# Performance work log

Hardware: AMD Instinct MI355X
Metric: run time of the kernel (lower is better)

## Reference

```python
import jax, jax.numpy as jnp
import numpy as np

EPS = 1e-5

def _ln(x, g, b):
    mu = jnp.mean(x, axis=-1, keepdims=True)
    var = jnp.mean((x - mu) ** 2, axis=-1, keepdims=True)
    return (x - mu) * jax.lax.rsqrt(var + EPS) * g + b

B, SQ, SK, C, H = 4, 1024, 2048, 1024, 16
DH = C // H          # head_dim (latent_dim == in_dim)
L = C                # latent_dim

def setup_inputs() -> dict:
    key = jax.random.key(0)
    ks = list(jax.random.split(key, 16))
    s = 0.02
    d = {
        'queries': jax.random.normal(ks[0], (B, SQ, C), jnp.float32),
        'contexts': jax.random.normal(ks[1], (B, SK, C), jnp.float32),
        # SelfAttention params
        'sa_ln_g': jnp.ones((C,), jnp.float32),
        'sa_ln_b': jnp.zeros((C,), jnp.float32),
        'sa_qkv_w': jax.random.normal(ks[2], (2 * L + C, C), jnp.float32) * s,  # torch Linear weight (out,in)
        'sa_out_w': jax.random.normal(ks[3], (C, C), jnp.float32) * s,
        'sa_out_b': jnp.zeros((C,), jnp.float32),
        # Cross Attention params
        'ca_ln_g': jnp.ones((C,), jnp.float32),
        'ca_ln_b': jnp.zeros((C,), jnp.float32),
        'ca_q_w': jax.random.normal(ks[4], (L, C), jnp.float32) * s,
        'ca_k_w': jax.random.normal(ks[5], (L, C), jnp.float32) * s,
        'ca_v_w': jax.random.normal(ks[6], (C, C), jnp.float32) * s,
        'ca_out_w': jax.random.normal(ks[7], (C, C), jnp.float32) * s,
        'ca_out_b': jnp.zeros((C,), jnp.float32),
        # FFN (linear block) params
        'ff_ln1_g': jnp.ones((C,), jnp.float32),
        'ff_ln1_b': jnp.zeros((C,), jnp.float32),
        'ff_w1': jax.random.normal(ks[8], (2 * C, C), jnp.float32) * s,
        'ff_ln2_g': jnp.ones((2 * C,), jnp.float32),
        'ff_ln2_b': jnp.zeros((2 * C,), jnp.float32),
        'ff_w2': jax.random.normal(ks[9], (C, 2 * C), jnp.float32) * s,
    }
    return d

def _forward(queries, contexts, sa_ln_g, sa_ln_b, sa_qkv_w, sa_out_w, sa_out_b,
             ca_ln_g, ca_ln_b, ca_q_w, ca_k_w, ca_v_w, ca_out_w, ca_out_b,
             ff_ln1_g, ff_ln1_b, ff_w1, ff_ln2_g, ff_ln2_b, ff_w2):
    scale = 1.0 / jnp.sqrt(jnp.float32(C))  # note: module scales by sqrt(C), not sqrt(head_dim)
    # ---- SelfAttention ----
    x = queries
    h = _ln(x, sa_ln_g, sa_ln_b)
    qkv = (h @ sa_qkv_w.T).reshape(B, SQ, H, -1)  # (B,SQ,H, 2*DH + C//H)
    q, k, v = jnp.split(qkv, [DH, 2 * DH], axis=-1)
    e = jnp.einsum('nqhc,nkhc->nhqk', q, k)
    a = jax.nn.softmax(e * scale, axis=-1)
    o = jnp.einsum('nhql,nlhc->nqhc', a, v).reshape(B, SQ, C)
    x = o @ sa_out_w.T + sa_out_b + x
    # ---- Cross Attention ----
    qpre = x
    hq = _ln(x, ca_ln_g, ca_ln_b)
    q = (hq @ ca_q_w.T).reshape(B, SQ, H, DH)
    k = (contexts @ ca_k_w.T).reshape(B, SK, H, DH)
    v = (contexts @ ca_v_w.T).reshape(B, SK, H, C // H)
    energy = jnp.einsum('nqhc,nkhc->nhqk', q, k)  # (B,H,SQ,SK)
    a = jax.nn.softmax(energy * scale, axis=-1)
    o = jnp.einsum('nhql,nlhc->nqhc', a, v).reshape(B, SQ, C)
    x = o @ ca_out_w.T + ca_out_b + qpre
    # ---- FFN: LN -> SiLU -> Linear -> LN -> SiLU -> Linear, residual ----
    f = jax.nn.silu(_ln(x, ff_ln1_g, ff_ln1_b))
    f = f @ ff_w1.T
    f = jax.nn.silu(_ln(f, ff_ln2_g, ff_ln2_b))
    f = f @ ff_w2.T
    out = x + f  # dropout p=0 -> identity
    return out, energy

def reference(queries, contexts, sa_ln_g, sa_ln_b, sa_qkv_w, sa_out_w, sa_out_b,
              ca_ln_g, ca_ln_b, ca_q_w, ca_k_w, ca_v_w, ca_out_w, ca_out_b,
              ff_ln1_g, ff_ln1_b, ff_w1, ff_ln2_g, ff_ln2_b, ff_w2):
    return _forward(queries, contexts, sa_ln_g, sa_ln_b, sa_qkv_w, sa_out_w, sa_out_b,
                    ca_ln_g, ca_ln_b, ca_q_w, ca_k_w, ca_v_w, ca_out_w, ca_out_b,
                    ff_ln1_g, ff_ln1_b, ff_w1, ff_ln2_g, ff_ln2_b, ff_w2)
```

## Files before the change

kernel.cpp:

```cpp
#include <hip/hip_runtime.h>
#include <hip/hip_bf16.h>
#include <math.h>


namespace {
constexpr int BB  = 4;
constexpr int SQ_ = 1024;
constexpr int SK_ = 2048;
constexpr int CC  = 1024;
constexpr int HH  = 16;
constexpr float SCALE  = 0.03125f;
constexpr float LN_EPS = 1e-5f;
constexpr size_t OPART_STRIDE = (size_t)BB * SQ_ * CC;
}

typedef __hip_bfloat16 bf16;
typedef __attribute__((ext_vector_type(8))) short short8;
typedef __attribute__((ext_vector_type(4))) float f32x4;

__device__ __forceinline__ void gload16(const void* g, void* l) {
    __builtin_amdgcn_global_load_lds((const __attribute__((address_space(1))) unsigned int*)g,
                                     (__attribute__((address_space(3))) unsigned int*)l,
                                     16, 0, 0);
}

__global__ __launch_bounds__(256)
void cvt_bf16(const float* __restrict__ in, bf16* __restrict__ out, int n8) {
    const int i = blockIdx.x * 256 + threadIdx.x;
    if (i >= n8) return;
    const float4 a = ((const float4*)in)[2 * i];
    const float4 b = ((const float4*)in)[2 * i + 1];
    union { ushort4 v; bf16 h[4]; } lo, hi;
    lo.h[0] = __float2bfloat16(a.x); lo.h[1] = __float2bfloat16(a.y);
    lo.h[2] = __float2bfloat16(a.z); lo.h[3] = __float2bfloat16(a.w);
    hi.h[0] = __float2bfloat16(b.x); hi.h[1] = __float2bfloat16(b.y);
    hi.h[2] = __float2bfloat16(b.z); hi.h[3] = __float2bfloat16(b.w);
    ((ushort4*)out)[2 * i]     = lo.v;
    ((ushort4*)out)[2 * i + 1] = hi.v;
}

template<int NCOLS>
__global__ __launch_bounds__(256)
void ln_kernel(const float* __restrict__ x, const float* __restrict__ g,
               const float* __restrict__ b, bf16* __restrict__ out, int do_silu) {
    constexpr int PER = NCOLS / 256;
    const size_t row = blockIdx.x;
    const float* xr = x + row * NCOLS;
    float vals[PER];
    float s = 0.f, ss = 0.f;
#pragma unroll
    for (int i = 0; i < PER; ++i) {
        vals[i] = xr[threadIdx.x + i * 256];
        s += vals[i];
        ss += vals[i] * vals[i];
    }
    for (int off = 32; off > 0; off >>= 1) {
        s  += __shfl_down(s, off, 64);
        ss += __shfl_down(ss, off, 64);
    }
    __shared__ float red[10];
    const int wid = threadIdx.x >> 6, lane = threadIdx.x & 63;
    if (lane == 0) { red[wid] = s; red[wid + 4] = ss; }
    __syncthreads();
    if (threadIdx.x == 0) {
        const float ts  = red[0] + red[1] + red[2] + red[3];
        const float tss = red[4] + red[5] + red[6] + red[7];
        const float mu  = ts / NCOLS;
        const float var = tss / NCOLS - mu * mu;
        red[8] = mu;
        red[9] = rsqrtf(var + LN_EPS);
    }
    __syncthreads();
    const float mu = red[8], rstd = red[9];
    bf16* outr = out + row * NCOLS;
#pragma unroll
    for (int i = 0; i < PER; ++i) {
        const int c = threadIdx.x + i * 256;
        float y = (vals[i] - mu) * rstd * g[c] + b[c];
        if (do_silu) y = y / (1.f + __expf(-y));
        outr[c] = __float2bfloat16(y);
    }
}

template<int OUT16>
__global__ __launch_bounds__(256)
void gemm_bt16(const bf16* __restrict__ A, const bf16* __restrict__ B,
               void* __restrict__ Cv, int M, int N, int K,
               const float* __restrict__ bias, const float* __restrict__ resid) {
    __shared__ bf16 As[128 * 32];
    __shared__ bf16 Bs[128 * 32];
    const int tid  = threadIdx.x;
    const int lane = tid & 63;
    const int w    = tid >> 6;
    const int wr = w >> 1, wc = w & 1;

    const int nwg = gridDim.x * gridDim.y;
    const int bid = blockIdx.x + gridDim.x * blockIdx.y;
    const int logical = (bid & 7) * (nwg >> 3) + (bid >> 3);
    const int m0 = (logical / gridDim.x) * 128;
    const int n0 = (logical % gridDim.x) * 128;

    f32x4 acc[4][4] = {};

    const int srow = tid >> 2;
    const int scol = (tid & 3) * 8;
    const bf16* Ap  = A + (size_t)(m0 + srow) * K + scol;
    const bf16* Ap2 = Ap + (size_t)64 * K;
    const bf16* Bp  = B + (size_t)(n0 + srow) * K + scol;
    const bf16* Bp2 = Bp + (size_t)64 * K;

    char* AsB = (char*)As + w * 1024;
    char* BsB = (char*)Bs + w * 1024;

    const int arow = wr * 64 + (lane & 15);
    const int brow = wc * 64 + (lane & 15);
    const int kgrp = (lane >> 4) * 16;

    for (int k0 = 0; k0 < K; k0 += 32) {
        gload16(Ap  + k0, AsB);
        gload16(Ap2 + k0, AsB + 4096);
        gload16(Bp  + k0, BsB);
        gload16(Bp2 + k0, BsB + 4096);
        __syncthreads();
        short8 aF[4], bF[4];
#pragma unroll
        for (int m = 0; m < 4; ++m)
            aF[m] = *(const short8*)((const char*)As + ((arow + m * 16) * 64 + kgrp));
#pragma unroll
        for (int n = 0; n < 4; ++n)
            bF[n] = *(const short8*)((const char*)Bs + ((brow + n * 16) * 64 + kgrp));
#pragma unroll
        for (int m = 0; m < 4; ++m)
#pragma unroll
            for (int n = 0; n < 4; ++n)
                acc[m][n] = __builtin_amdgcn_mfma_f32_16x16x32_bf16(aF[m], bF[n], acc[m][n], 0, 0, 0);
        __syncthreads();
    }

    const int crow0 = m0 + wr * 64 + (lane >> 4) * 4;
    const int ccol0 = n0 + wc * 64 + (lane & 15);
#pragma unroll
    for (int m = 0; m < 4; ++m) {
#pragma unroll
        for (int n = 0; n < 4; ++n) {
            const int col = ccol0 + n * 16;
            const float bv = (!OUT16 && bias) ? bias[col] : 0.f;
#pragma unroll
            for (int j = 0; j < 4; ++j) {
                const int row = crow0 + m * 16 + j;
                float v = acc[m][n][j] + bv;
                if (!OUT16 && resid) v += resid[(size_t)row * N + col];
                if (OUT16) ((bf16*)Cv)[(size_t)row * N + col] = __float2bfloat16(v);
                else       ((float*)Cv)[(size_t)row * N + col] = v;
            }
        }
    }
}

__global__ __launch_bounds__(256)
void transpose_v(const bf16* __restrict__ X, int ldx, int cs, int co,
                 bf16* __restrict__ T, int ldt) {
    __shared__ bf16 t[64][66];
    const int r0 = blockIdx.x * 64, c0 = blockIdx.y * 64;
#pragma unroll
    for (int s = 0; s < 16; ++s) {
        const int r = (threadIdx.x >> 6) + s * 4;
        const int c = threadIdx.x & 63;
        const int cc = c0 + c;
        t[r][c] = X[(size_t)(r0 + r) * ldx + (size_t)(cc >> 6) * cs + co + (cc & 63)];
    }
    __syncthreads();
#pragma unroll
    for (int s = 0; s < 16; ++s) {
        const int c = (threadIdx.x >> 6) + s * 4;
        const int r = threadIdx.x & 63;
        T[(size_t)(c0 + c) * ldt + r0 + r] = t[r][c];
    }
}

template<bool ENERGY, int NSPLIT>
__global__ __launch_bounds__(256, 4)
void flash_attn(const bf16* __restrict__ Qb, int ldq, int qh_str,
                const bf16* __restrict__ Kb, int ldk, int kh_str, int kh_add,
                const bf16* __restrict__ Vt, int ldvt,
                bf16* __restrict__ O, float* __restrict__ Opart,
                float* __restrict__ stats, float* __restrict__ energy,
                int SKV, int SQl, float scale) {
    __shared__ bf16 P[64][136];
    const int tid = threadIdx.x;
    const int lane = tid & 63, wid = tid >> 6;
    const int l15 = lane & 15, l4 = lane >> 4;

    const int gx  = gridDim.x;
    const int nwg = gx * gridDim.y * gridDim.z;
    const int bid = blockIdx.x + gx * (blockIdx.y + gridDim.y * blockIdx.z);
    const int logical = (bid & 7) * (nwg >> 3) + (bid >> 3);
    const int xq = logical % gx;
    const int z  = (logical / gx) % (BB * HH);
    const int split = (NSPLIT > 1) ? (logical / (gx * BB * HH)) : 0;

    const int b = z >> 4, h = z & 15;
    const int q0 = xq * 64;
    const int kv_begin = split * (SKV / NSPLIT);
    const int kv_end   = kv_begin + SKV / NSPLIT;

    const bf16* Qp = Qb + (size_t)b * SQl * ldq + (size_t)h * qh_str;
    const bf16* Kp = Kb + (size_t)b * SKV * ldk + (size_t)h * kh_str + kh_add;
    const bf16* Vp = Vt + (size_t)h * 64 * ldvt + (size_t)b * SKV;

    short8 aQ[2];
#pragma unroll
    for (int s = 0; s < 2; ++s)
        aQ[s] = *(const short8*)(Qp + (size_t)(q0 + wid * 16 + l15) * ldq + s * 32 + l4 * 8);

    f32x4 oacc[4] = {};
    float mI = -1e30f, lI = 0.f;

    for (int kv0 = kv_begin; kv0 < kv_end; kv0 += 64) {
        f32x4 sa[4] = {};
#pragma unroll
        for (int n = 0; n < 4; ++n) {
            const bf16* kr = Kp + (size_t)(kv0 + n * 16 + l15) * ldk + l4 * 8;
            const short8 b0 = *(const short8*)(kr);
            const short8 b1 = *(const short8*)(kr + 32);
            sa[n] = __builtin_amdgcn_mfma_f32_16x16x32_bf16(b0, aQ[0], sa[n], 0, 0, 0);
            sa[n] = __builtin_amdgcn_mfma_f32_16x16x32_bf16(b1, aQ[1], sa[n], 0, 0, 0);
        }
        if (ENERGY) {
            float* er = energy + (size_t)z * SQl * SKV
                      + (size_t)(q0 + wid * 16 + l15) * SKV + kv0 + l4 * 4;
#pragma unroll
            for (int n = 0; n < 4; ++n)
                __builtin_nontemporal_store(sa[n], (f32x4*)(er + n * 16));
        }
        float mx = fmaxf(fmaxf(fmaxf(sa[0][0], sa[0][1]), fmaxf(sa[0][2], sa[0][3])),
                         fmaxf(fmaxf(sa[1][0], sa[1][1]), fmaxf(sa[1][2], sa[1][3])));
        mx = fmaxf(mx, fmaxf(fmaxf(sa[2][0], sa[2][1]), fmaxf(sa[2][2], sa[2][3])));
        mx = fmaxf(mx, fmaxf(fmaxf(sa[3][0], sa[3][1]), fmaxf(sa[3][2], sa[3][3])));
        mx *= scale;
        mx = fmaxf(mx, __shfl_xor(mx, 16, 64));
        mx = fmaxf(mx, __shfl_xor(mx, 32, 64));
        const float nm = fmaxf(mI, mx);
        const float f = __expf(mI - nm);
        mI = nm;
        float rs = 0.f;
#pragma unroll
        for (int n = 0; n < 4; ++n)
#pragma unroll
            for (int j = 0; j < 4; ++j) {
                const float p = __expf(sa[n][j] * scale - nm);
                sa[n][j] = p;
                rs += p;
            }
        rs += __shfl_xor(rs, 16, 64);
        rs += __shfl_xor(rs, 32, 64);
        lI = lI * f + rs;
#pragma unroll
        for (int j = 0; j < 4; ++j) {
            const float fj = __shfl(f, l4 * 4 + j, 64);
#pragma unroll
            for (int n = 0; n < 4; ++n) oacc[n][j] *= fj;
        }
#pragma unroll
        for (int n = 0; n < 4; ++n) {
            union { ushort4 v; bf16 hh[4]; } pk;
            pk.hh[0] = __float2bfloat16(sa[n][0]);
            pk.hh[1] = __float2bfloat16(sa[n][1]);
            pk.hh[2] = __float2bfloat16(sa[n][2]);
            pk.hh[3] = __float2bfloat16(sa[n][3]);
            *(ushort4*)(&P[wid * 16 + l15][n * 16 + l4 * 4]) = pk.v;
        }
#pragma unroll
        for (int ks = 0; ks < 2; ++ks) {
            const short8 aP = *(const short8*)(&P[wid * 16 + l15][ks * 32 + l4 * 8]);
#pragma unroll
            for (int n = 0; n < 4; ++n) {
                const short8 bV = *(const short8*)(Vp + (size_t)(n * 16 + l15) * ldvt + kv0 + ks * 32 + l4 * 8);
                oacc[n] = __builtin_amdgcn_mfma_f32_16x16x32_bf16(aP, bV, oacc[n], 0, 0, 0);
            }
        }
    }
    if (NSPLIT == 1) {
#pragma unroll
        for (int j = 0; j < 4; ++j) {
            const float lj = __shfl(lI, l4 * 4 + j, 64);
            const float rl = 1.f / lj;
            const size_t row = (size_t)b * SQl + q0 + wid * 16 + l4 * 4 + j;
#pragma unroll
            for (int n = 0; n < 4; ++n)
                O[row * 1024 + h * 64 + n * 16 + l15] = __float2bfloat16(oacc[n][j] * rl);
        }
    } else {
        float* Op = Opart + (size_t)split * OPART_STRIDE;
#pragma unroll
        for (int j = 0; j < 4; ++j) {
            const size_t row = (size_t)b * SQl + q0 + wid * 16 + l4 * 4 + j;
#pragma unroll
            for (int n = 0; n < 4; ++n)
                Op[row * 1024 + h * 64 + n * 16 + l15] = oacc[n][j];
        }
        if (l4 == 0) {
            float2* st = (float2*)stats;
            st[((size_t)split * BB * HH + z) * SQl + q0 + wid * 16 + l15] =
                make_float2(mI, lI);
        }
    }
}

__global__ __launch_bounds__(256)
void merge_o(const float* __restrict__ Opart, const float* __restrict__ stats,
             bf16* __restrict__ O) {
    const size_t row = blockIdx.x;
    const int b = (int)(row >> 10), q = (int)(row & 1023);
    const int col = threadIdx.x * 4;
    const int h = col >> 6;
    const int zi = b * HH + h;
    const float2* st = (const float2*)stats;
    const float2 s1 = st[(size_t)zi * SQ_ + q];
    const float2 s2 = st[((size_t)BB * HH + zi) * SQ_ + q];
    const float m = fmaxf(s1.x, s2.x);
    const float w1 = __expf(s1.x - m), w2 = __expf(s2.x - m);
    const float invl = 1.f / (s1.y * w1 + s2.y * w2);
    const float4 o1 = *(const float4*)(Opart + row * 1024 + col);
    const float4 o2 = *(const float4*)(Opart + OPART_STRIDE + row * 1024 + col);
    union { ushort4 v; bf16 hh[4]; } r;
    r.hh[0] = __float2bfloat16((o1.x * w1 + o2.x * w2) * invl);
    r.hh[1] = __float2bfloat16((o1.y * w1 + o2.y * w2) * invl);
    r.hh[2] = __float2bfloat16((o1.z * w1 + o2.z * w2) * invl);
    r.hh[3] = __float2bfloat16((o1.w * w1 + o2.w * w2) * invl);
    *(ushort4*)(O + row * 1024 + col) = r.v;
}

extern "C" void kernel_launch(void* const* d_in, const int* in_sizes, int n_in,
                              void* d_out, int out_size, void* d_ws, size_t ws_size,
                              hipStream_t stream) {
    const float* queries  = (const float*)d_in[0];
    const float* contexts = (const float*)d_in[1];
    const float* sa_ln_g  = (const float*)d_in[2];
    const float* sa_ln_b  = (const float*)d_in[3];
    const float* sa_qkv_w = (const float*)d_in[4];
    const float* sa_out_w = (const float*)d_in[5];
    const float* sa_out_b = (const float*)d_in[6];
    const float* ca_ln_g  = (const float*)d_in[7];
    const float* ca_ln_b  = (const float*)d_in[8];
    const float* ca_q_w   = (const float*)d_in[9];
    const float* ca_k_w   = (const float*)d_in[10];
    const float* ca_v_w   = (const float*)d_in[11];
    const float* ca_out_w = (const float*)d_in[12];
    const float* ca_out_b = (const float*)d_in[13];
    const float* ff_ln1_g = (const float*)d_in[14];
    const float* ff_ln1_b = (const float*)d_in[15];
    const float* ff_w1    = (const float*)d_in[16];
    const float* ff_ln2_g = (const float*)d_in[17];
    const float* ff_ln2_b = (const float*)d_in[18];
    const float* ff_w2    = (const float*)d_in[19];

    float* out    = (float*)d_out;
    float* energy = out + (size_t)BB * SQ_ * CC;

    const size_t MEG = 1024 * 1024;

    float* ws = (float*)d_ws;
    bf16*  X0_16      = (bf16*)ws;
    bf16*  o16        = (bf16*)(ws + 4 * MEG);
    bf16*  ca_out_w16 = (bf16*)(ws + 6 * MEG);
    bf16*  ff_w1_16   = (bf16*)(ws + (13 * MEG) / 2);
    bf16*  ff_w2_16   = (bf16*)(ws + (15 * MEG) / 2);
    bf16*  q_ca16     = (bf16*)(ws + (17 * MEG) / 2);
    bf16*  k_ca16     = (bf16*)(ws + (21 * MEG) / 2);
    bf16*  Vt_ca      = (bf16*)(ws + (29 * MEG) / 2);
    float* E_buf      = ws + (37 * MEG) / 2;
    float* C_buf      = ws + (45 * MEG) / 2;
    bf16*  v_ca16     = (bf16*)C_buf;
    float* Opart      = C_buf;
    float* stats_buf  = ws + (61 * MEG) / 2;

    bf16* EZ         = (bf16*)energy;
    bf16* ctx16      = EZ;
    bf16* qkv16      = EZ + 8  * MEG;
    bf16* Vt_sa      = EZ + 20 * MEG;
    bf16* qkv_w16    = EZ + 24 * MEG;
    bf16* sa_out_w16 = EZ + 27 * MEG;
    bf16* ca_q_w16   = EZ + 28 * MEG;
    bf16* ca_k_w16   = EZ + 29 * MEG;
    bf16* ca_v_w16   = EZ + 30 * MEG;

    const int M1 = BB * SQ_;
    const int M2 = BB * SK_;
    const dim3 thr(256);
    auto cvt = [&](const float* src, bf16* dst, size_t n) {
        int n8 = (int)(n / 8);
        cvt_bf16<<<(n8 + 255) / 256, thr, 0, stream>>>(src, dst, n8);
    };

    cvt(sa_qkv_w, qkv_w16,    3 * MEG);
    cvt(sa_out_w, sa_out_w16, 1 * MEG);
    cvt(ca_q_w,   ca_q_w16,   1 * MEG);
    cvt(ca_k_w,   ca_k_w16,   1 * MEG);
    cvt(ca_v_w,   ca_v_w16,   1 * MEG);
    cvt(ca_out_w, ca_out_w16, 1 * MEG);
    cvt(ff_w1,    ff_w1_16,   2 * MEG);
    cvt(ff_w2,    ff_w2_16,   2 * MEG);
    cvt(contexts, ctx16,      8 * MEG);

    ln_kernel<1024><<<M1, thr, 0, stream>>>(queries, sa_ln_g, sa_ln_b, X0_16, 0);
    gemm_bt16<1><<<dim3(3072 / 128, M1 / 128), thr, 0, stream>>>(X0_16, qkv_w16, qkv16,
                                                                 M1, 3072, 1024, nullptr, nullptr);
    transpose_v<<<dim3(M1 / 64, 1024 / 64), thr, 0, stream>>>(qkv16, 3072, 192, 128, Vt_sa, M1);
    flash_attn<false, 1><<<dim3(SQ_ / 64, BB * HH, 1), thr, 0, stream>>>(
        qkv16, 3072, 192, qkv16, 3072, 192, 64, Vt_sa, M1,
        o16, nullptr, nullptr, nullptr, SQ_, SQ_, SCALE);
    gemm_bt16<0><<<dim3(1024 / 128, M1 / 128), thr, 0, stream>>>(o16, sa_out_w16, E_buf,
                                                                 M1, CC, CC, sa_out_b, queries);

    ln_kernel<1024><<<M1, thr, 0, stream>>>(E_buf, ca_ln_g, ca_ln_b, X0_16, 0);
    gemm_bt16<1><<<dim3(1024 / 128, M1 / 128), thr, 0, stream>>>(X0_16, ca_q_w16, q_ca16,
                                                                 M1, CC, CC, nullptr, nullptr);
    gemm_bt16<1><<<dim3(1024 / 128, M2 / 128), thr, 0, stream>>>(ctx16, ca_k_w16, k_ca16,
                                                                 M2, CC, CC, nullptr, nullptr);
    gemm_bt16<1><<<dim3(1024 / 128, M2 / 128), thr, 0, stream>>>(ctx16, ca_v_w16, v_ca16,
                                                                 M2, CC, CC, nullptr, nullptr);
    transpose_v<<<dim3(M2 / 64, 1024 / 64), thr, 0, stream>>>(v_ca16, 1024, 64, 0, Vt_ca, M2);
    flash_attn<true, 2><<<dim3(SQ_ / 64, BB * HH, 2), thr, 0, stream>>>(
        q_ca16, 1024, 64, k_ca16, 1024, 64, 0, Vt_ca, M2,
        nullptr, Opart, stats_buf, energy, SK_, SQ_, SCALE);
    merge_o<<<M1, thr, 0, stream>>>(Opart, stats_buf, o16);
    gemm_bt16<0><<<dim3(1024 / 128, M1 / 128), thr, 0, stream>>>(o16, ca_out_w16, E_buf,
                                                                 M1, CC, CC, ca_out_b, E_buf);

    ln_kernel<1024><<<M1, thr, 0, stream>>>(E_buf, ff_ln1_g, ff_ln1_b, X0_16, 1);
    gemm_bt16<0><<<dim3(2048 / 128, M1 / 128), thr, 0, stream>>>(X0_16, ff_w1_16, C_buf,
                                                                 M1, 2048, 1024, nullptr, nullptr);
    ln_kernel<2048><<<M1, thr, 0, stream>>>(C_buf, ff_ln2_g, ff_ln2_b, X0_16, 1);
    gemm_bt16<0><<<dim3(1024 / 128, M1 / 128), thr, 0, stream>>>(X0_16, ff_w2_16, out,
                                                                 M1, CC, 2048, nullptr, E_buf);
}
```

Measured before the change: 760.0 us.

## Batch conversions, double-buffer GEMM, fuse K/V projection, drop attention KV split

Replaces nine bf16 conversion launches with one job-table kernel, double-buffers LDS tiles in the GEMM so the next tile's loads are issued before computing the current one, and merges the cross-attention K and V projections into a single GEMM using adjacent weight buffers. It also removes the two-way KV split and merge kernel in cross-attention, writing normalized output directly. This cuts launches and intermediate traffic but halves attention parallelism, and prefetching into LDS without an explicit wait before use may risk ordering issues.

```diff
diff --git a/kernel.cpp b/kernel.cpp
--- a/kernel.cpp
+++ b/kernel.cpp
@@ -11,7 +11,6 @@
 constexpr int HH  = 16;
 constexpr float SCALE  = 0.03125f;
 constexpr float LN_EPS = 1e-5f;
-constexpr size_t OPART_STRIDE = (size_t)BB * SQ_ * CC;
 }
 
 typedef __hip_bfloat16 bf16;
@@ -24,19 +23,31 @@
                                      16, 0, 0);
 }
 
+#define MAXJOBS 10
+struct CvtJobs {
+    const float* src[MAXJOBS];
+    bf16*        dst[MAXJOBS];
+    int          end[MAXJOBS];
+    int          njobs;
+};
+
 __global__ __launch_bounds__(256)
-void cvt_bf16(const float* __restrict__ in, bf16* __restrict__ out, int n8) {
+void cvt_all(CvtJobs J) {
     const int i = blockIdx.x * 256 + threadIdx.x;
-    if (i >= n8) return;
-    const float4 a = ((const float4*)in)[2 * i];
-    const float4 b = ((const float4*)in)[2 * i + 1];
+    if (i >= J.end[J.njobs - 1]) return;
+    int j = 0;
+    while (i >= J.end[j]) ++j;
+    const int base = j ? J.end[j - 1] : 0;
+    const int k = i - base;
+    const float4 a = ((const float4*)J.src[j])[2 * k];
+    const float4 b = ((const float4*)J.src[j])[2 * k + 1];
     union { ushort4 v; bf16 h[4]; } lo, hi;
     lo.h[0] = __float2bfloat16(a.x); lo.h[1] = __float2bfloat16(a.y);
     lo.h[2] = __float2bfloat16(a.z); lo.h[3] = __float2bfloat16(a.w);
     hi.h[0] = __float2bfloat16(b.x); hi.h[1] = __float2bfloat16(b.y);
     hi.h[2] = __float2bfloat16(b.z); hi.h[3] = __float2bfloat16(b.w);
-    ((ushort4*)out)[2 * i]     = lo.v;
-    ((ushort4*)out)[2 * i + 1] = hi.v;
+    ((ushort4*)J.dst[j])[2 * k]     = lo.v;
+    ((ushort4*)J.dst[j])[2 * k + 1] = hi.v;
 }
 
 template<int NCOLS>
@@ -87,8 +98,8 @@
 void gemm_bt16(const bf16* __restrict__ A, const bf16* __restrict__ B,
                void* __restrict__ Cv, int M, int N, int K,
                const float* __restrict__ bias, const float* __restrict__ resid) {
-    __shared__ bf16 As[128 * 32];
-    __shared__ bf16 Bs[128 * 32];
+    __shared__ bf16 As[2][128 * 32];
+    __shared__ bf16 Bs[2][128 * 32];
     const int tid  = threadIdx.x;
     const int lane = tid & 63;
     const int w    = tid >> 6;
@@ -109,26 +120,33 @@
     const bf16* Bp  = B + (size_t)(n0 + srow) * K + scol;
     const bf16* Bp2 = Bp + (size_t)64 * K;
 
-    char* AsB = (char*)As + w * 1024;
-    char* BsB = (char*)Bs + w * 1024;
-
     const int arow = wr * 64 + (lane & 15);
     const int brow = wc * 64 + (lane & 15);
     const int kgrp = (lane >> 4) * 16;
 
-    for (int k0 = 0; k0 < K; k0 += 32) {
+    auto stage = [&](int buf, int k0) {
+        char* AsB = (char*)As[buf] + w * 1024;
+        char* BsB = (char*)Bs[buf] + w * 1024;
         gload16(Ap  + k0, AsB);
         gload16(Ap2 + k0, AsB + 4096);
         gload16(Bp  + k0, BsB);
         gload16(Bp2 + k0, BsB + 4096);
-        __syncthreads();
+    };
+
+    const int nt = K >> 5;
+    stage(0, 0);
+    __syncthreads();
+    for (int t = 0; t < nt; ++t) {
+        if (t + 1 < nt) stage((t + 1) & 1, (t + 1) << 5);
+        const char* Ab = (const char*)As[t & 1];
+        const char* Bb = (const char*)Bs[t & 1];
         short8 aF[4], bF[4];
 #pragma unroll
         for (int m = 0; m < 4; ++m)
-            aF[m] = *(const short8*)((const char*)As + ((arow + m * 16) * 64 + kgrp));
+            aF[m] = *(const short8*)(Ab + ((arow + m * 16) * 64 + kgrp));
 #pragma unroll
         for (int n = 0; n < 4; ++n)
-            bF[n] = *(const short8*)((const char*)Bs + ((brow + n * 16) * 64 + kgrp));
+            bF[n] = *(const short8*)(Bb + ((brow + n * 16) * 64 + kgrp));
 #pragma unroll
         for (int m = 0; m < 4; ++m)
 #pragma unroll
@@ -178,13 +196,12 @@
     }
 }
 
-template<bool ENERGY, int NSPLIT>
+template<bool ENERGY>
 __global__ __launch_bounds__(256, 4)
 void flash_attn(const bf16* __restrict__ Qb, int ldq, int qh_str,
                 const bf16* __restrict__ Kb, int ldk, int kh_str, int kh_add,
                 const bf16* __restrict__ Vt, int ldvt,
-                bf16* __restrict__ O, float* __restrict__ Opart,
-                float* __restrict__ stats, float* __restrict__ energy,
+                bf16* __restrict__ O, float* __restrict__ energy,
                 int SKV, int SQl, float scale) {
     __shared__ bf16 P[64][136];
     const int tid = threadIdx.x;
@@ -192,17 +209,14 @@
     const int l15 = lane & 15, l4 = lane >> 4;
 
     const int gx  = gridDim.x;
-    const int nwg = gx * gridDim.y * gridDim.z;
-    const int bid = blockIdx.x + gx * (blockIdx.y + gridDim.y * blockIdx.z);
+    const int nwg = gx * gridDim.y;
+    const int bid = blockIdx.x + gx * blockIdx.y;
     const int logical = (bid & 7) * (nwg >> 3) + (bid >> 3);
     const int xq = logical % gx;
-    const int z  = (logical / gx) % (BB * HH);
-    const int split = (NSPLIT > 1) ? (logical / (gx * BB * HH)) : 0;
+    const int z  = logical / gx;
 
     const int b = z >> 4, h = z & 15;
     const int q0 = xq * 64;
-    const int kv_begin = split * (SKV / NSPLIT);
-    const int kv_end   = kv_begin + SKV / NSPLIT;
 
     const bf16* Qp = Qb + (size_t)b * SQl * ldq + (size_t)h * qh_str;
     const bf16* Kp = Kb + (size_t)b * SKV * ldk + (size_t)h * kh_str + kh_add;
@@ -216,7 +230,7 @@
     f32x4 oacc[4] = {};
     float mI = -1e30f, lI = 0.f;
 
-    for (int kv0 = kv_begin; kv0 < kv_end; kv0 += 64) {
+    for (int kv0 = 0; kv0 < SKV; kv0 += 64) {
         f32x4 sa[4] = {};
 #pragma unroll
         for (int n = 0; n < 4; ++n) {
@@ -280,55 +294,15 @@
             }
         }
     }
-    if (NSPLIT == 1) {
-#pragma unroll
-        for (int j = 0; j < 4; ++j) {
-            const float lj = __shfl(lI, l4 * 4 + j, 64);
-            const float rl = 1.f / lj;
-            const size_t row = (size_t)b * SQl + q0 + wid * 16 + l4 * 4 + j;
-#pragma unroll
-            for (int n = 0; n < 4; ++n)
-                O[row * 1024 + h * 64 + n * 16 + l15] = __float2bfloat16(oacc[n][j] * rl);
-        }
-    } else {
-        float* Op = Opart + (size_t)split * OPART_STRIDE;
-#pragma unroll
-        for (int j = 0; j < 4; ++j) {
-            const size_t row = (size_t)b * SQl + q0 + wid * 16 + l4 * 4 + j;
-#pragma unroll
-            for (int n = 0; n < 4; ++n)
-                Op[row * 1024 + h * 64 + n * 16 + l15] = oacc[n][j];
-        }
-        if (l4 == 0) {
-            float2* st = (float2*)stats;
-            st[((size_t)split * BB * HH + z) * SQl + q0 + wid * 16 + l15] =
-                make_float2(mI, lI);
-        }
-    }
-}
-
-__global__ __launch_bounds__(256)
-void merge_o(const float* __restrict__ Opart, const float* __restrict__ stats,
-             bf16* __restrict__ O) {
-    const size_t row = blockIdx.x;
-    const int b = (int)(row >> 10), q = (int)(row & 1023);
-    const int col = threadIdx.x * 4;
-    const int h = col >> 6;
-    const int zi = b * HH + h;
-    const float2* st = (const float2*)stats;
-    const float2 s1 = st[(size_t)zi * SQ_ + q];
-    const float2 s2 = st[((size_t)BB * HH + zi) * SQ_ + q];
-    const float m = fmaxf(s1.x, s2.x);
-    const float w1 = __expf(s1.x - m), w2 = __expf(s2.x - m);
-    const float invl = 1.f / (s1.y * w1 + s2.y * w2);
-    const float4 o1 = *(const float4*)(Opart + row * 1024 + col);
-    const float4 o2 = *(const float4*)(Opart + OPART_STRIDE + row * 1024 + col);
-    union { ushort4 v; bf16 hh[4]; } r;
-    r.hh[0] = __float2bfloat16((o1.x * w1 + o2.x * w2) * invl);
-    r.hh[1] = __float2bfloat16((o1.y * w1 + o2.y * w2) * invl);
-    r.hh[2] = __float2bfloat16((o1.z * w1 + o2.z * w2) * invl);
-    r.hh[3] = __float2bfloat16((o1.w * w1 + o2.w * w2) * invl);
-    *(ushort4*)(O + row * 1024 + col) = r.v;
+#pragma unroll
+    for (int j = 0; j < 4; ++j) {
+        const float lj = __shfl(lI, l4 * 4 + j, 64);
+        const float rl = 1.f / lj;
+        const size_t row = (size_t)b * SQl + q0 + wid * 16 + l4 * 4 + j;
+#pragma unroll
+        for (int n = 0; n < 4; ++n)
+            O[row * 1024 + h * 64 + n * 16 + l15] = __float2bfloat16(oacc[n][j] * rl);
+    }
 }
 
 extern "C" void kernel_launch(void* const* d_in, const int* in_sizes, int n_in,
@@ -367,13 +341,10 @@
     bf16*  ff_w1_16   = (bf16*)(ws + (13 * MEG) / 2);
     bf16*  ff_w2_16   = (bf16*)(ws + (15 * MEG) / 2);
     bf16*  q_ca16     = (bf16*)(ws + (17 * MEG) / 2);
-    bf16*  k_ca16     = (bf16*)(ws + (21 * MEG) / 2);
-    bf16*  Vt_ca      = (bf16*)(ws + (29 * MEG) / 2);
-    float* E_buf      = ws + (37 * MEG) / 2;
-    float* C_buf      = ws + (45 * MEG) / 2;
-    bf16*  v_ca16     = (bf16*)C_buf;
-    float* Opart      = C_buf;
-    float* stats_buf  = ws + (61 * MEG) / 2;
+    bf16*  KV_ca      = (bf16*)(ws + (21 * MEG) / 2);
+    bf16*  Vt_ca      = (bf16*)(ws + (37 * MEG) / 2);
+    float* E_buf      = ws + (45 * MEG) / 2;
+    float* C_buf      = ws + (53 * MEG) / 2;
 
     bf16* EZ         = (bf16*)energy;
     bf16* ctx16      = EZ;
@@ -388,43 +359,45 @@
     const int M1 = BB * SQ_;
     const int M2 = BB * SK_;
     const dim3 thr(256);
-    auto cvt = [&](const float* src, bf16* dst, size_t n) {
-        int n8 = (int)(n / 8);
-        cvt_bf16<<<(n8 + 255) / 256, thr, 0, stream>>>(src, dst, n8);
-    };
-
-    cvt(sa_qkv_w, qkv_w16,    3 * MEG);
-    cvt(sa_out_w, sa_out_w16, 1 * MEG);
-    cvt(ca_q_w,   ca_q_w16,   1 * MEG);
-    cvt(ca_k_w,   ca_k_w16,   1 * MEG);
-    cvt(ca_v_w,   ca_v_w16,   1 * MEG);
-    cvt(ca_out_w, ca_out_w16, 1 * MEG);
-    cvt(ff_w1,    ff_w1_16,   2 * MEG);
-    cvt(ff_w2,    ff_w2_16,   2 * MEG);
-    cvt(contexts, ctx16,      8 * MEG);
+
+    {
+        CvtJobs J;
+        const float* srcs[9] = { sa_qkv_w, sa_out_w, ca_q_w, ca_k_w, ca_v_w,
+                                 ca_out_w, ff_w1, ff_w2, contexts };
+        bf16* dsts[9] = { qkv_w16, sa_out_w16, ca_q_w16, ca_k_w16, ca_v_w16,
+                          ca_out_w16, ff_w1_16, ff_w2_16, ctx16 };
+        const size_t ns[9] = { 3 * MEG, 1 * MEG, 1 * MEG, 1 * MEG, 1 * MEG,
+                               1 * MEG, 2 * MEG, 2 * MEG, 8 * MEG };
+        int acc_n8 = 0;
+        for (int j = 0; j < 9; ++j) {
+            J.src[j] = srcs[j];
+            J.dst[j] = dsts[j];
+            acc_n8 += (int)(ns[j] / 8);
+            J.end[j] = acc_n8;
+        }
+        J.njobs = 9;
+        cvt_all<<<(acc_n8 + 255) / 256, thr, 0, stream>>>(J);
+    }
 
     ln_kernel<1024><<<M1, thr, 0, stream>>>(queries, sa_ln_g, sa_ln_b, X0_16, 0);
     gemm_bt16<1><<<dim3(3072 / 128, M1 / 128), thr, 0, stream>>>(X0_16, qkv_w16, qkv16,
                                                                  M1, 3072, 1024, nullptr, nullptr);
     transpose_v<<<dim3(M1 / 64, 1024 / 64), thr, 0, stream>>>(qkv16, 3072, 192, 128, Vt_sa, M1);
-    flash_attn<false, 1><<<dim3(SQ_ / 64, BB * HH, 1), thr, 0, stream>>>(
+    flash_attn<false><<<dim3(SQ_ / 64, BB * HH), thr, 0, stream>>>(
         qkv16, 3072, 192, qkv16, 3072, 192, 64, Vt_sa, M1,
-        o16, nullptr, nullptr, nullptr, SQ_, SQ_, SCALE);
+        o16, nullptr, SQ_, SQ_, SCALE);
     gemm_bt16<0><<<dim3(1024 / 128, M1 / 128), thr, 0, stream>>>(o16, sa_out_w16, E_buf,
                                                                  M1, CC, CC, sa_out_b, queries);
 
     ln_kernel<1024><<<M1, thr, 0, stream>>>(E_buf, ca_ln_g, ca_ln_b, X0_16, 0);
     gemm_bt16<1><<<dim3(1024 / 128, M1 / 128), thr, 0, stream>>>(X0_16, ca_q_w16, q_ca16,
                                                                  M1, CC, CC, nullptr, nullptr);
-    gemm_bt16<1><<<dim3(1024 / 128, M2 / 128), thr, 0, stream>>>(ctx16, ca_k_w16, k_ca16,
-                                                                 M2, CC, CC, nullptr, nullptr);
-    gemm_bt16<1><<<dim3(1024 / 128, M2 / 128), thr, 0, stream>>>(ctx16, ca_v_w16, v_ca16,
-                                                                 M2, CC, CC, nullptr, nullptr);
-    transpose_v<<<dim3(M2 / 64, 1024 / 64), thr, 0, stream>>>(v_ca16, 1024, 64, 0, Vt_ca, M2);
-    flash_attn<true, 2><<<dim3(SQ_ / 64, BB * HH, 2), thr, 0, stream>>>(
-        q_ca16, 1024, 64, k_ca16, 1024, 64, 0, Vt_ca, M2,
-        nullptr, Opart, stats_buf, energy, SK_, SQ_, SCALE);
-    merge_o<<<M1, thr, 0, stream>>>(Opart, stats_buf, o16);
+    gemm_bt16<1><<<dim3(2048 / 128, M2 / 128), thr, 0, stream>>>(ctx16, ca_k_w16, KV_ca,
+                                                                 M2, 2048, 1024, nullptr, nullptr);
+    transpose_v<<<dim3(M2 / 64, 1024 / 64), thr, 0, stream>>>(KV_ca, 2048, 64, 1024, Vt_ca, M2);
+    flash_attn<true><<<dim3(SQ_ / 64, BB * HH), thr, 0, stream>>>(
+        q_ca16, 1024, 64, KV_ca, 2048, 64, 0, Vt_ca, M2,
+        o16, energy, SK_, SQ_, SCALE);
     gemm_bt16<0><<<dim3(1024 / 128, M1 / 128), thr, 0, stream>>>(o16, ca_out_w16, E_buf,
                                                                  M1, CC, CC, ca_out_b, E_buf);
 
```

Result: faster. 714.2 us (-6.0%).
